# Kernel tuning notes

Measured on AMD Instinct MI355X. Metric: run time of the kernel, lower is better.

Reference implementation:

```python
import jax, jax.numpy as jnp
import numpy as np

N_NODES = 20000
N_EDGES = 320000
IN_F = 256
OUT_F = 64
HEADS = 4
ALPHA = 0.1  # leaky_relu negative slope


def setup_inputs() -> dict:
    key = jax.random.key(0)
    ks = jax.random.split(key, 8)
    return {
        "input1": jax.random.normal(ks[0], (N_NODES, IN_F), jnp.float32),
        "input2": jax.random.normal(ks[1], (N_NODES, IN_F), jnp.float32),
        # per-head params: Ws maps source feats -> target_out, Wt maps target feats -> source_out
        "Ws": jax.random.normal(ks[2], (HEADS, IN_F, OUT_F), jnp.float32) * 0.06,
        "Wt": jax.random.normal(ks[3], (HEADS, IN_F, OUT_F), jnp.float32) * 0.06,
        "a1": jax.random.normal(ks[4], (HEADS, 2 * OUT_F), jnp.float32) * 0.1,
        "a2": jax.random.normal(ks[5], (HEADS, 2 * OUT_F), jnp.float32) * 0.1,
        # COO nonzeros of A_opt [n_target, n_source]
        "tgt_idx": jax.random.randint(ks[6], (N_EDGES,), 0, N_NODES),
        "src_idx": jax.random.randint(ks[7], (N_EDGES,), 0, N_NODES),
    }


def _segment_softmax(scores, seg, num_segments):
    m = jax.lax.stop_gradient(jax.ops.segment_max(scores, seg, num_segments=num_segments))
    w = jnp.exp(scores - m[seg])
    d = jax.ops.segment_sum(w, seg, num_segments=num_segments)
    d = jnp.where(d == 0, 1.0, d)
    return w / d[seg]


def _head(x1, x2, Ws, Wt, a1, a2, src, tgt, n_s, n_t):
    s = x1 @ Ws  # [n_s, OUT_F]  messages source -> target
    t = x2 @ Wt  # [n_t, OUT_F]  messages target -> source
    out = Ws.shape[1]
    # edge score e = leaky_relu(a^T [s_src || t_tgt]); split a to avoid edge-level concat
    e1 = jax.nn.leaky_relu((s @ a1[:out])[src] + (t @ a1[out:])[tgt], ALPHA)
    e2 = jax.nn.leaky_relu((s @ a2[:out])[src] + (t @ a2[out:])[tgt], ALPHA)
    alpha_ts = _segment_softmax(e1, tgt, n_t)  # softmax over sources per target
    alpha_st = _segment_softmax(e2, src, n_s)  # softmax over targets per source
    h_ts = jax.ops.segment_sum(alpha_ts[:, None] * s[src], tgt, num_segments=n_t)
    h_st = jax.ops.segment_sum(alpha_st[:, None] * t[tgt], src, num_segments=n_s)
    return jax.nn.elu(h_st), jax.nn.elu(h_ts)  # concat=True -> ELU per head


def reference(input1, input2, Ws, Wt, a1, a2, tgt_idx, src_idx):
    n_s, n_t = input1.shape[0], input2.shape[0]
    head_fn = jax.vmap(
        lambda W1, W2, v1, v2: _head(input1, input2, W1, W2, v1, v2, src_idx, tgt_idx, n_s, n_t)
    )
    h_st, h_ts = head_fn(Ws, Wt, a1, a2)  # each [H, n, OUT_F]
    h_st = jnp.transpose(h_st, (1, 0, 2)).reshape(n_s, -1)  # concat heads
    h_ts = jnp.transpose(h_ts, (1, 0, 2)).reshape(n_t, -1)
    return h_st, h_ts
```

## Files before the change

### kernel.cpp

```cpp
#include <hip/hip_runtime.h>
#include <math.h>

#define N_NODES 20000
#define N_EDGES 320000
#define IN_F 256
#define OUT_F 64
#define HEADS 4
#define NCOL 256
#define LRELU_ALPHA 0.1f
#define ELL_CAP 64

#define SCAT_X 64
#define SCAT_THREADS (SCAT_X * 2 * 256)
#define GEMM_BX 625

typedef __attribute__((ext_vector_type(8))) short short8;
typedef __attribute__((ext_vector_type(4))) float floatx4;

__device__ __forceinline__ float lrelu(float x) {
    return x > 0.f ? x : LRELU_ALPHA * x;
}
__device__ __forceinline__ unsigned short f2bf(float f) {
    unsigned int u = __float_as_uint(f);
    u = (u + 0x7FFF + ((u >> 16) & 1)) >> 16;
    return (unsigned short)u;
}
__device__ __forceinline__ float bf2f(unsigned short u) {
    return __uint_as_float(((unsigned int)u) << 16);
}

__global__ __launch_bounds__(256) void prep_w_kernel(
    const float* __restrict__ Ws, const float* __restrict__ Wt,
    unsigned short* __restrict__ Wsb, unsigned short* __restrict__ Wtb,
    int* __restrict__ cnt)
{
    const int gid = blockIdx.x * 256 + threadIdx.x;

    for (int i = gid; i < 2 * N_NODES; i += 16384) cnt[i] = 0;

    const int mat = gid >> 13;
    const int r   = gid & 8191;
    const int kc  = r >> 8;
    const int c   = r & 255;
    const float* W    = mat ? Wt : Ws;
    unsigned short* O = mat ? Wtb : Wsb;
    const int h = c >> 6, j = c & 63;
    const int k0 = kc * 8;
    unsigned short v[8] __attribute__((aligned(16)));
#pragma unroll
    for (int i = 0; i < 8; ++i)
        v[i] = f2bf(W[(size_t)h * (IN_F * OUT_F) + (size_t)(k0 + i) * OUT_F + j]);
    *(uint4*)(O + (size_t)c * IN_F + k0) = *(const uint4*)v;
}

__device__ __forceinline__ void scat_one(
    int e, const int* __restrict__ src, const int* __restrict__ tgt,
    int* __restrict__ cnt_t, int* __restrict__ cnt_s,
    int* __restrict__ elist_t, int* __restrict__ elist_s)
{
    int sn = src[e], tn = tgt[e];
    int p = atomicAdd(&cnt_t[tn], 1);
    if (p < ELL_CAP) elist_t[tn * ELL_CAP + p] = sn;
    int q = atomicAdd(&cnt_s[sn], 1);
    if (q < ELL_CAP) elist_s[sn * ELL_CAP + q] = tn;
}

__global__ __launch_bounds__(256) void gemm_hybrid_kernel(
    const float* __restrict__ A0, const unsigned short* __restrict__ Wb0,
    const float* __restrict__ A1, const unsigned short* __restrict__ Wb1,
    unsigned short* __restrict__ C0, unsigned short* __restrict__ C1,
    const float* __restrict__ a1, const float* __restrict__ a2,
    float* __restrict__ ss1, float* __restrict__ ss2,
    float* __restrict__ tt1, float* __restrict__ tt2,
    const int* __restrict__ src, const int* __restrict__ tgt,
    int* __restrict__ cnt_t, int* __restrict__ cnt_s,
    int* __restrict__ elist_t, int* __restrict__ elist_s)
{
    const int tid = threadIdx.x;

    if (blockIdx.x < SCAT_X) {
        const int base = (blockIdx.y * SCAT_X + blockIdx.x) * 256 + tid;
        int e = base;
        for (; e + 3 * SCAT_THREADS < N_EDGES; e += 4 * SCAT_THREADS) {
            int e0 = e, e1 = e + SCAT_THREADS, e2 = e + 2 * SCAT_THREADS, e3 = e + 3 * SCAT_THREADS;
            int s0 = src[e0], t0 = tgt[e0];
            int s1 = src[e1], t1 = tgt[e1];
            int s2 = src[e2], t2 = tgt[e2];
            int s3 = src[e3], t3 = tgt[e3];
            int p0 = atomicAdd(&cnt_t[t0], 1);
            int q0 = atomicAdd(&cnt_s[s0], 1);
            int p1 = atomicAdd(&cnt_t[t1], 1);
            int q1 = atomicAdd(&cnt_s[s1], 1);
            int p2 = atomicAdd(&cnt_t[t2], 1);
            int q2 = atomicAdd(&cnt_s[s2], 1);
            int p3 = atomicAdd(&cnt_t[t3], 1);
            int q3 = atomicAdd(&cnt_s[s3], 1);
            if (p0 < ELL_CAP) elist_t[t0 * ELL_CAP + p0] = s0;
            if (q0 < ELL_CAP) elist_s[s0 * ELL_CAP + q0] = t0;
            if (p1 < ELL_CAP) elist_t[t1 * ELL_CAP + p1] = s1;
            if (q1 < ELL_CAP) elist_s[s1 * ELL_CAP + q1] = t1;
            if (p2 < ELL_CAP) elist_t[t2 * ELL_CAP + p2] = s2;
            if (q2 < ELL_CAP) elist_s[s2 * ELL_CAP + q2] = t2;
            if (p3 < ELL_CAP) elist_t[t3 * ELL_CAP + p3] = s3;
            if (q3 < ELL_CAP) elist_s[s3 * ELL_CAP + q3] = t3;
        }
        for (; e < N_EDGES; e += SCAT_THREADS)
            scat_one(e, src, tgt, cnt_t, cnt_s, elist_t, elist_s);
        return;
    }

    const int bx = blockIdx.x - SCAT_X;
    const float* A           = (blockIdx.y == 0) ? A0 : A1;
    const unsigned short* Wb = (blockIdx.y == 0) ? Wb0 : Wb1;
    unsigned short* C        = (blockIdx.y == 0) ? C0 : C1;

    __shared__ __align__(16) unsigned short Bl[256][40];

    const int lane  = tid & 63;
    const int w     = tid >> 6;
    const int quad  = lane >> 4;
    const int l15   = lane & 15;
    const int mhalf = w & 1, nhalf = w >> 1;
    const int r0    = bx * 32;
    const int mrow  = r0 + mhalf * 16 + l15;

    floatx4 acc[8];
#pragma unroll
    for (int t = 0; t < 8; ++t) acc[t] = (floatx4){0.f, 0.f, 0.f, 0.f};

    const float* arow = A + (size_t)mrow * IN_F + quad * 8;

    for (int k0 = 0; k0 < IN_F; k0 += 32) {
#pragma unroll
        for (int p = 0; p < 4; ++p) {
            int idx = p * 256 + tid;
            int n = idx >> 2, kc = idx & 3;
            uint4 v = *(const uint4*)(Wb + (size_t)n * 256 + k0 + kc * 8);
            *(uint4*)&Bl[n][kc * 8] = v;
        }
        __syncthreads();

        float4 av0 = *(const float4*)(arow + k0);
        float4 av1 = *(const float4*)(arow + k0 + 4);
        short8 afrag;
        afrag[0] = (short)f2bf(av0.x); afrag[1] = (short)f2bf(av0.y);
        afrag[2] = (short)f2bf(av0.z); afrag[3] = (short)f2bf(av0.w);
        afrag[4] = (short)f2bf(av1.x); afrag[5] = (short)f2bf(av1.y);
        afrag[6] = (short)f2bf(av1.z); afrag[7] = (short)f2bf(av1.w);

#pragma unroll
        for (int t = 0; t < 8; ++t) {
            int n = (nhalf * 8 + t) * 16 + l15;
            short8 bfrag = *(const short8*)&Bl[n][quad * 8];
            acc[t] = __builtin_amdgcn_mfma_f32_16x16x32_bf16(afrag, bfrag, acc[t], 0, 0, 0);
        }
        __syncthreads();
    }

#pragma unroll
    for (int t = 0; t < 8; ++t) {
        int col = (nhalf * 8 + t) * 16 + l15;
#pragma unroll
        for (int r = 0; r < 4; ++r) {
            int m = r0 + mhalf * 16 + quad * 4 + r;
            C[(size_t)m * NCOL + col] = f2bf(acc[t][r]);
        }
    }

    const int off_aj = (blockIdx.y == 0) ? 0 : 64;
    float* o1 = (blockIdx.y == 0) ? ss1 : tt1;
    float* o2 = (blockIdx.y == 0) ? ss2 : tt2;

    float p1[2][4] = {{0.f,0.f,0.f,0.f},{0.f,0.f,0.f,0.f}};
    float p2[2][4] = {{0.f,0.f,0.f,0.f},{0.f,0.f,0.f,0.f}};
#pragma unroll
    for (int t = 0; t < 8; ++t) {
        int hh = 2 * nhalf + (t >> 2);
        int jj = ((t & 3) * 16) + l15;
        float w1 = a1[hh * 128 + off_aj + jj];
        float w2 = a2[hh * 128 + off_aj + jj];
        int a = t >> 2;
#pragma unroll
        for (int r = 0; r < 4; ++r) {
            p1[a][r] += acc[t][r] * w1;
            p2[a][r] += acc[t][r] * w2;
        }
    }
#pragma unroll
    for (int m = 1; m < 16; m <<= 1) {
#pragma unroll
        for (int a = 0; a < 2; ++a)
#pragma unroll
            for (int r = 0; r < 4; ++r) {
                p1[a][r] += __shfl_xor(p1[a][r], m, 64);
                p2[a][r] += __shfl_xor(p2[a][r], m, 64);
            }
    }
    if (l15 == 0) {
#pragma unroll
        for (int r = 0; r < 4; ++r) {
            int m = r0 + mhalf * 16 + quad * 4 + r;
#pragma unroll
            for (int a = 0; a < 2; ++a) {
                int hh = 2 * nhalf + a;
                o1[m * HEADS + hh] = p1[a][r];
                o2[m * HEADS + hh] = p2[a][r];
            }
        }
    }
}

__global__ __launch_bounds__(256) void agg_kernel(
    const int* __restrict__ cnt_t, const int* __restrict__ elist_t,
    const int* __restrict__ cnt_s, const int* __restrict__ elist_s,
    const float* __restrict__ ss1, const float* __restrict__ ss2,
    const float* __restrict__ tt1, const float* __restrict__ tt2,
    const unsigned short* __restrict__ s_bf, const unsigned short* __restrict__ t_bf,
    float* __restrict__ h_st, float* __restrict__ h_ts)
{
    const int wave = threadIdx.x >> 6;
    const int lane = threadIdx.x & 63;
    const int n    = blockIdx.x * 4 + wave;
    const int dir  = blockIdx.y;
    const int h    = lane >> 4;
    const int coff = lane * 4;

    const int*            cnt   = dir ? cnt_s   : cnt_t;
    const int*            list  = dir ? elist_s : elist_t;
    const unsigned short* table = dir ? t_bf    : s_bf;
    const float*          nsc   = dir ? ss2     : tt1;
    const float*          esc   = dir ? tt2     : ss1;
    float*                outp  = dir ? h_st    : h_ts;

    const float base = nsc[n * HEADS + h];
    int deg = cnt[n];
    if (deg > ELL_CAP) deg = ELL_CAP;
    const int b0 = n * ELL_CAP, b1 = b0 + deg;

    float4 acc = make_float4(0.f, 0.f, 0.f, 0.f);
    float den = 0.f;

    int p = b0;
    for (; p + 3 < b1; p += 4) {
        int m0 = list[p],     m1 = list[p + 1];
        int m2 = list[p + 2], m3 = list[p + 3];
        float e0 = esc[m0 * HEADS + h], e1 = esc[m1 * HEADS + h];
        float e2 = esc[m2 * HEADS + h], e3 = esc[m3 * HEADS + h];
        ushort4 r0 = *(const ushort4*)(table + (size_t)m0 * NCOL + coff);
        ushort4 r1 = *(const ushort4*)(table + (size_t)m1 * NCOL + coff);
        ushort4 r2 = *(const ushort4*)(table + (size_t)m2 * NCOL + coff);
        ushort4 r3 = *(const ushort4*)(table + (size_t)m3 * NCOL + coff);
        float w0 = __expf(lrelu(e0 + base));
        float w1 = __expf(lrelu(e1 + base));
        float w2 = __expf(lrelu(e2 + base));
        float w3 = __expf(lrelu(e3 + base));
        den += (w0 + w1) + (w2 + w3);
        acc.x += (w0 * bf2f(r0.x) + w1 * bf2f(r1.x)) + (w2 * bf2f(r2.x) + w3 * bf2f(r3.x));
        acc.y += (w0 * bf2f(r0.y) + w1 * bf2f(r1.y)) + (w2 * bf2f(r2.y) + w3 * bf2f(r3.y));
        acc.z += (w0 * bf2f(r0.z) + w1 * bf2f(r1.z)) + (w2 * bf2f(r2.z) + w3 * bf2f(r3.z));
        acc.w += (w0 * bf2f(r0.w) + w1 * bf2f(r1.w)) + (w2 * bf2f(r2.w) + w3 * bf2f(r3.w));
    }
    for (; p < b1; ++p) {
        int m0 = list[p];
        float w0 = __expf(lrelu(esc[m0 * HEADS + h] + base));
        ushort4 r0 = *(const ushort4*)(table + (size_t)m0 * NCOL + coff);
        den += w0;
        acc.x += w0 * bf2f(r0.x);
        acc.y += w0 * bf2f(r0.y);
        acc.z += w0 * bf2f(r0.z);
        acc.w += w0 * bf2f(r0.w);
    }

    if (den == 0.f) den = 1.f;
    float inv = 1.f / den;
    float4 r;
    r.x = acc.x * inv; r.y = acc.y * inv; r.z = acc.z * inv; r.w = acc.w * inv;
    r.x = (r.x > 0.f) ? r.x : expm1f(r.x);
    r.y = (r.y > 0.f) ? r.y : expm1f(r.y);
    r.z = (r.z > 0.f) ? r.z : expm1f(r.z);
    r.w = (r.w > 0.f) ? r.w : expm1f(r.w);
    *(float4*)(outp + (size_t)n * NCOL + coff) = r;
}

extern "C" void kernel_launch(void* const* d_in, const int* in_sizes, int n_in,
                              void* d_out, int out_size, void* d_ws, size_t ws_size,
                              hipStream_t stream)
{
    const float* input1 = (const float*)d_in[0];
    const float* input2 = (const float*)d_in[1];
    const float* Ws     = (const float*)d_in[2];
    const float* Wt     = (const float*)d_in[3];
    const float* a1     = (const float*)d_in[4];
    const float* a2     = (const float*)d_in[5];
    const int*   tgt    = (const int*)d_in[6];
    const int*   src    = (const int*)d_in[7];

    float* out  = (float*)d_out;
    float* h_st = out;
    float* h_ts = out + (size_t)N_NODES * NCOL;

    unsigned short* s_bf = (unsigned short*)d_ws;
    unsigned short* t_bf = s_bf + (size_t)N_NODES * NCOL;
    unsigned short* Wsb  = t_bf + (size_t)N_NODES * NCOL;
    unsigned short* Wtb  = Wsb + 256 * 256;
    float* ss1  = (float*)(Wtb + 256 * 256);
    float* ss2  = ss1 + N_NODES * HEADS;
    float* tt1  = ss2 + N_NODES * HEADS;
    float* tt2  = tt1 + N_NODES * HEADS;
    int*   cnt_t = (int*)(tt2 + N_NODES * HEADS);
    int*   cnt_s = cnt_t + N_NODES;
    int*   elist_t = cnt_s + N_NODES;
    int*   elist_s = elist_t + N_NODES * ELL_CAP;

    prep_w_kernel<<<64, 256, 0, stream>>>(Ws, Wt, Wsb, Wtb, cnt_t);

    dim3 ggrid(SCAT_X + GEMM_BX, 2);
    gemm_hybrid_kernel<<<ggrid, 256, 0, stream>>>(input1, Wsb, input2, Wtb,
                                                  s_bf, t_bf, a1, a2,
                                                  ss1, ss2, tt1, tt2,
                                                  src, tgt, cnt_t, cnt_s,
                                                  elist_t, elist_s);

    dim3 agrid(N_NODES / 4, 2);
    agg_kernel<<<agrid, 256, 0, stream>>>(cnt_t, elist_t, cnt_s, elist_s,
                                          ss1, ss2, tt1, tt2, s_bf, t_bf, h_st, h_ts);
}
```

Before: 192.0 us.

## Split scatter into its own kernel, keep full W in LDS, shrink edge lists to u16

The edge scatter moves out of the fused GEMM into a separate kernel with one pass of two edges per thread. The GEMM becomes a persistent kernel: each 512-thread block loads the whole 256x256 bf16 weight into padded LDS once, then each wave loops over 16-row tiles and computes all 256 columns, which removes the per-k-step weight reloads and barriers. ELL edge lists are stored as 16-bit node indices, halving their write and read traffic. In exchange, the scatter and GEMM no longer overlap, and the large LDS footprint limits how many blocks fit per CU.

```diff
diff --git a/kernel.cpp b/kernel.cpp
--- a/kernel.cpp
+++ b/kernel.cpp
@@ -10,9 +10,11 @@
 #define LRELU_ALPHA 0.1f
 #define ELL_CAP 64
 
-#define SCAT_X 64
-#define SCAT_THREADS (SCAT_X * 2 * 256)
-#define GEMM_BX 625
+#define SCAT_BLOCKS 640
+#define SCAT_THREADS (SCAT_BLOCKS * 256)
+
+#define WRES_BLOCKS 128
+#define LDS_STRIDE 264
 
 typedef __attribute__((ext_vector_type(8))) short short8;
 typedef __attribute__((ext_vector_type(4))) float floatx4;
@@ -53,166 +55,147 @@
     *(uint4*)(O + (size_t)c * IN_F + k0) = *(const uint4*)v;
 }
 
-__device__ __forceinline__ void scat_one(
-    int e, const int* __restrict__ src, const int* __restrict__ tgt,
+__global__ __launch_bounds__(256) void scatter_kernel(
+    const int* __restrict__ src, const int* __restrict__ tgt,
     int* __restrict__ cnt_t, int* __restrict__ cnt_s,
-    int* __restrict__ elist_t, int* __restrict__ elist_s)
-{
-    int sn = src[e], tn = tgt[e];
-    int p = atomicAdd(&cnt_t[tn], 1);
-    if (p < ELL_CAP) elist_t[tn * ELL_CAP + p] = sn;
-    int q = atomicAdd(&cnt_s[sn], 1);
-    if (q < ELL_CAP) elist_s[sn * ELL_CAP + q] = tn;
-}
-
-__global__ __launch_bounds__(256) void gemm_hybrid_kernel(
+    unsigned short* __restrict__ elist_t, unsigned short* __restrict__ elist_s)
+{
+    const int e0 = blockIdx.x * 256 + threadIdx.x;
+    const int e1 = e0 + SCAT_THREADS;
+    const bool h1 = e1 < N_EDGES;
+
+    int s0 = src[e0], t0 = tgt[e0];
+    int s1 = 0, t1 = 0;
+    if (h1) { s1 = src[e1]; t1 = tgt[e1]; }
+
+    int p0 = atomicAdd(&cnt_t[t0], 1);
+    int q0 = atomicAdd(&cnt_s[s0], 1);
+    int p1 = 0, q1 = 0;
+    if (h1) {
+        p1 = atomicAdd(&cnt_t[t1], 1);
+        q1 = atomicAdd(&cnt_s[s1], 1);
+    }
+
+    if (p0 < ELL_CAP) elist_t[t0 * ELL_CAP + p0] = (unsigned short)s0;
+    if (q0 < ELL_CAP) elist_s[s0 * ELL_CAP + q0] = (unsigned short)t0;
+    if (h1) {
+        if (p1 < ELL_CAP) elist_t[t1 * ELL_CAP + p1] = (unsigned short)s1;
+        if (q1 < ELL_CAP) elist_s[s1 * ELL_CAP + q1] = (unsigned short)t1;
+    }
+}
+
+__global__ __launch_bounds__(512, 2) void gemm_wres_kernel(
     const float* __restrict__ A0, const unsigned short* __restrict__ Wb0,
     const float* __restrict__ A1, const unsigned short* __restrict__ Wb1,
     unsigned short* __restrict__ C0, unsigned short* __restrict__ C1,
     const float* __restrict__ a1, const float* __restrict__ a2,
     float* __restrict__ ss1, float* __restrict__ ss2,
-    float* __restrict__ tt1, float* __restrict__ tt2,
-    const int* __restrict__ src, const int* __restrict__ tgt,
-    int* __restrict__ cnt_t, int* __restrict__ cnt_s,
-    int* __restrict__ elist_t, int* __restrict__ elist_s)
+    float* __restrict__ tt1, float* __restrict__ tt2)
 {
     const int tid = threadIdx.x;
-
-    if (blockIdx.x < SCAT_X) {
-        const int base = (blockIdx.y * SCAT_X + blockIdx.x) * 256 + tid;
-        int e = base;
-        for (; e + 3 * SCAT_THREADS < N_EDGES; e += 4 * SCAT_THREADS) {
-            int e0 = e, e1 = e + SCAT_THREADS, e2 = e + 2 * SCAT_THREADS, e3 = e + 3 * SCAT_THREADS;
-            int s0 = src[e0], t0 = tgt[e0];
-            int s1 = src[e1], t1 = tgt[e1];
-            int s2 = src[e2], t2 = tgt[e2];
-            int s3 = src[e3], t3 = tgt[e3];
-            int p0 = atomicAdd(&cnt_t[t0], 1);
-            int q0 = atomicAdd(&cnt_s[s0], 1);
-            int p1 = atomicAdd(&cnt_t[t1], 1);
-            int q1 = atomicAdd(&cnt_s[s1], 1);
-            int p2 = atomicAdd(&cnt_t[t2], 1);
-            int q2 = atomicAdd(&cnt_s[s2], 1);
-            int p3 = atomicAdd(&cnt_t[t3], 1);
-            int q3 = atomicAdd(&cnt_s[s3], 1);
-            if (p0 < ELL_CAP) elist_t[t0 * ELL_CAP + p0] = s0;
-            if (q0 < ELL_CAP) elist_s[s0 * ELL_CAP + q0] = t0;
-            if (p1 < ELL_CAP) elist_t[t1 * ELL_CAP + p1] = s1;
-            if (q1 < ELL_CAP) elist_s[s1 * ELL_CAP + q1] = t1;
-            if (p2 < ELL_CAP) elist_t[t2 * ELL_CAP + p2] = s2;
-            if (q2 < ELL_CAP) elist_s[s2 * ELL_CAP + q2] = t2;
-            if (p3 < ELL_CAP) elist_t[t3 * ELL_CAP + p3] = s3;
-            if (q3 < ELL_CAP) elist_s[s3 * ELL_CAP + q3] = t3;
-        }
-        for (; e < N_EDGES; e += SCAT_THREADS)
-            scat_one(e, src, tgt, cnt_t, cnt_s, elist_t, elist_s);
-        return;
-    }
-
-    const int bx = blockIdx.x - SCAT_X;
     const float* A           = (blockIdx.y == 0) ? A0 : A1;
     const unsigned short* Wb = (blockIdx.y == 0) ? Wb0 : Wb1;
     unsigned short* C        = (blockIdx.y == 0) ? C0 : C1;
 
-    __shared__ __align__(16) unsigned short Bl[256][40];
-
-    const int lane  = tid & 63;
-    const int w     = tid >> 6;
-    const int quad  = lane >> 4;
-    const int l15   = lane & 15;
-    const int mhalf = w & 1, nhalf = w >> 1;
-    const int r0    = bx * 32;
-    const int mrow  = r0 + mhalf * 16 + l15;
-
-    floatx4 acc[8];
-#pragma unroll
-    for (int t = 0; t < 8; ++t) acc[t] = (floatx4){0.f, 0.f, 0.f, 0.f};
-
-    const float* arow = A + (size_t)mrow * IN_F + quad * 8;
-
-    for (int k0 = 0; k0 < IN_F; k0 += 32) {
-#pragma unroll
-        for (int p = 0; p < 4; ++p) {
-            int idx = p * 256 + tid;
-            int n = idx >> 2, kc = idx & 3;
-            uint4 v = *(const uint4*)(Wb + (size_t)n * 256 + k0 + kc * 8);
-            *(uint4*)&Bl[n][kc * 8] = v;
-        }
-        __syncthreads();
-
-        float4 av0 = *(const float4*)(arow + k0);
-        float4 av1 = *(const float4*)(arow + k0 + 4);
-        short8 afrag;
-        afrag[0] = (short)f2bf(av0.x); afrag[1] = (short)f2bf(av0.y);
-        afrag[2] = (short)f2bf(av0.z); afrag[3] = (short)f2bf(av0.w);
-        afrag[4] = (short)f2bf(av1.x); afrag[5] = (short)f2bf(av1.y);
-        afrag[6] = (short)f2bf(av1.z); afrag[7] = (short)f2bf(av1.w);
-
-#pragma unroll
-        for (int t = 0; t < 8; ++t) {
-            int n = (nhalf * 8 + t) * 16 + l15;
-            short8 bfrag = *(const short8*)&Bl[n][quad * 8];
-            acc[t] = __builtin_amdgcn_mfma_f32_16x16x32_bf16(afrag, bfrag, acc[t], 0, 0, 0);
-        }
-        __syncthreads();
-    }
-
-#pragma unroll
-    for (int t = 0; t < 8; ++t) {
-        int col = (nhalf * 8 + t) * 16 + l15;
-#pragma unroll
-        for (int r = 0; r < 4; ++r) {
-            int m = r0 + mhalf * 16 + quad * 4 + r;
-            C[(size_t)m * NCOL + col] = f2bf(acc[t][r]);
-        }
-    }
+    __shared__ __align__(16) unsigned short Bl[256][LDS_STRIDE];
+
+    for (int i = tid; i < 8192; i += 512) {
+        const int n  = i >> 5;
+        const int kc = (i & 31) << 3;
+        *(uint4*)&Bl[n][kc] = *(const uint4*)(Wb + (size_t)n * IN_F + kc);
+    }
+    __syncthreads();
+
+    const int lane = tid & 63;
+    const int w    = tid >> 6;
+    const int quad = lane >> 4;
+    const int l15  = lane & 15;
+    const int slot = blockIdx.x * 8 + w;
 
     const int off_aj = (blockIdx.y == 0) ? 0 : 64;
     float* o1 = (blockIdx.y == 0) ? ss1 : tt1;
     float* o2 = (blockIdx.y == 0) ? ss2 : tt2;
 
-    float p1[2][4] = {{0.f,0.f,0.f,0.f},{0.f,0.f,0.f,0.f}};
-    float p2[2][4] = {{0.f,0.f,0.f,0.f},{0.f,0.f,0.f,0.f}};
-#pragma unroll
-    for (int t = 0; t < 8; ++t) {
-        int hh = 2 * nhalf + (t >> 2);
-        int jj = ((t & 3) * 16) + l15;
-        float w1 = a1[hh * 128 + off_aj + jj];
-        float w2 = a2[hh * 128 + off_aj + jj];
-        int a = t >> 2;
-#pragma unroll
-        for (int r = 0; r < 4; ++r) {
-            p1[a][r] += acc[t][r] * w1;
-            p2[a][r] += acc[t][r] * w2;
-        }
-    }
-#pragma unroll
-    for (int m = 1; m < 16; m <<= 1) {
-#pragma unroll
-        for (int a = 0; a < 2; ++a)
+    for (int g = slot; g < 1250; g += 1024) {
+        const float* arow = A + (size_t)(g * 16 + l15) * IN_F + quad * 8;
+
+        short8 af[8];
+#pragma unroll
+        for (int kk = 0; kk < 8; ++kk) {
+            float4 u = *(const float4*)(arow + kk * 32);
+            float4 v = *(const float4*)(arow + kk * 32 + 4);
+            short8 t;
+            t[0] = (short)f2bf(u.x); t[1] = (short)f2bf(u.y);
+            t[2] = (short)f2bf(u.z); t[3] = (short)f2bf(u.w);
+            t[4] = (short)f2bf(v.x); t[5] = (short)f2bf(v.y);
+            t[6] = (short)f2bf(v.z); t[7] = (short)f2bf(v.w);
+            af[kk] = t;
+        }
+
+        floatx4 acc[16];
+#pragma unroll
+        for (int c = 0; c < 16; ++c) acc[c] = (floatx4){0.f, 0.f, 0.f, 0.f};
+
+#pragma unroll
+        for (int kk = 0; kk < 8; ++kk) {
+#pragma unroll
+            for (int c = 0; c < 16; ++c) {
+                short8 bfrag = *(const short8*)&Bl[c * 16 + l15][kk * 32 + quad * 8];
+                acc[c] = __builtin_amdgcn_mfma_f32_16x16x32_bf16(af[kk], bfrag, acc[c], 0, 0, 0);
+            }
+        }
+
+#pragma unroll
+        for (int c = 0; c < 16; ++c) {
+            const int col = c * 16 + l15;
 #pragma unroll
             for (int r = 0; r < 4; ++r) {
-                p1[a][r] += __shfl_xor(p1[a][r], m, 64);
-                p2[a][r] += __shfl_xor(p2[a][r], m, 64);
+                const int m = g * 16 + quad * 4 + r;
+                C[(size_t)m * NCOL + col] = f2bf(acc[c][r]);
             }
-    }
-    if (l15 == 0) {
-#pragma unroll
-        for (int r = 0; r < 4; ++r) {
-            int m = r0 + mhalf * 16 + quad * 4 + r;
-#pragma unroll
-            for (int a = 0; a < 2; ++a) {
-                int hh = 2 * nhalf + a;
-                o1[m * HEADS + hh] = p1[a][r];
-                o2[m * HEADS + hh] = p2[a][r];
+        }
+
+        float p1[4][4] = {{0.f,0.f,0.f,0.f},{0.f,0.f,0.f,0.f},{0.f,0.f,0.f,0.f},{0.f,0.f,0.f,0.f}};
+        float p2[4][4] = {{0.f,0.f,0.f,0.f},{0.f,0.f,0.f,0.f},{0.f,0.f,0.f,0.f},{0.f,0.f,0.f,0.f}};
+#pragma unroll
+        for (int c = 0; c < 16; ++c) {
+            const int hh = c >> 2;
+            const int jj = (c & 3) * 16 + l15;
+            const float w1 = a1[hh * 128 + off_aj + jj];
+            const float w2 = a2[hh * 128 + off_aj + jj];
+#pragma unroll
+            for (int r = 0; r < 4; ++r) {
+                p1[hh][r] += acc[c][r] * w1;
+                p2[hh][r] += acc[c][r] * w2;
             }
         }
+#pragma unroll
+        for (int m = 1; m < 16; m <<= 1) {
+#pragma unroll
+            for (int hh = 0; hh < 4; ++hh)
+#pragma unroll
+                for (int r = 0; r < 4; ++r) {
+                    p1[hh][r] += __shfl_xor(p1[hh][r], m, 64);
+                    p2[hh][r] += __shfl_xor(p2[hh][r], m, 64);
+                }
+        }
+        if (l15 == 0) {
+#pragma unroll
+            for (int r = 0; r < 4; ++r) {
+                const int m = g * 16 + quad * 4 + r;
+#pragma unroll
+                for (int hh = 0; hh < 4; ++hh) {
+                    o1[m * HEADS + hh] = p1[hh][r];
+                    o2[m * HEADS + hh] = p2[hh][r];
+                }
+            }
+        }
     }
 }
 
 __global__ __launch_bounds__(256) void agg_kernel(
-    const int* __restrict__ cnt_t, const int* __restrict__ elist_t,
-    const int* __restrict__ cnt_s, const int* __restrict__ elist_s,
+    const int* __restrict__ cnt_t, const unsigned short* __restrict__ elist_t,
+    const int* __restrict__ cnt_s, const unsigned short* __restrict__ elist_s,
     const float* __restrict__ ss1, const float* __restrict__ ss2,
     const float* __restrict__ tt1, const float* __restrict__ tt2,
     const unsigned short* __restrict__ s_bf, const unsigned short* __restrict__ t_bf,
@@ -226,7 +209,7 @@
     const int coff = lane * 4;
 
     const int*            cnt   = dir ? cnt_s   : cnt_t;
-    const int*            list  = dir ? elist_s : elist_t;
+    const unsigned short* list  = dir ? elist_s : elist_t;
     const unsigned short* table = dir ? t_bf    : s_bf;
     const float*          nsc   = dir ? ss2     : tt1;
     const float*          esc   = dir ? tt2     : ss1;
@@ -309,17 +292,18 @@
     float* tt2  = tt1 + N_NODES * HEADS;
     int*   cnt_t = (int*)(tt2 + N_NODES * HEADS);
     int*   cnt_s = cnt_t + N_NODES;
-    int*   elist_t = cnt_s + N_NODES;
-    int*   elist_s = elist_t + N_NODES * ELL_CAP;
+    unsigned short* elist_t = (unsigned short*)(cnt_s + N_NODES);
+    unsigned short* elist_s = elist_t + (size_t)N_NODES * ELL_CAP;
 
     prep_w_kernel<<<64, 256, 0, stream>>>(Ws, Wt, Wsb, Wtb, cnt_t);
 
-    dim3 ggrid(SCAT_X + GEMM_BX, 2);
-    gemm_hybrid_kernel<<<ggrid, 256, 0, stream>>>(input1, Wsb, input2, Wtb,
-                                                  s_bf, t_bf, a1, a2,
-                                                  ss1, ss2, tt1, tt2,
-                                                  src, tgt, cnt_t, cnt_s,
-                                                  elist_t, elist_s);
+    scatter_kernel<<<SCAT_BLOCKS, 256, 0, stream>>>(src, tgt, cnt_t, cnt_s,
+                                                    elist_t, elist_s);
+
+    dim3 ggrid(WRES_BLOCKS, 2);
+    gemm_wres_kernel<<<ggrid, 512, 0, stream>>>(input1, Wsb, input2, Wtb,
+                                                s_bf, t_bf, a1, a2,
+                                                ss1, ss2, tt1, tt2);
 
     dim3 agrid(N_NODES / 4, 2);
     agg_kernel<<<agrid, 256, 0, stream>>>(cnt_t, elist_t, cnt_s, elist_s,
```

Measured after the change: 193.6 us. No clear change (+0.9%).
